# Kernel optimization log

Hardware: AMD Instinct MI355X
Metric: run time of the kernel (lower is better)

Reference implementation:

```python
import jax, jax.numpy as jnp
import numpy as np

HS, WS = 64, 64
SIGMA = 1.2
UPDATE_COEFF = 0.2
R = 3
N_BLOCKS = 3
GROUPS = 8
EPS_GN = 1e-5
CM, CP, CS, CT, HID = 64, 3, 128, 128, 128
B, T, HIN, WIN = 32, 256, 128, 128


def setup_inputs() -> dict:
    key = jax.random.key(0)
    ks = jax.random.split(key, 10)
    s = 0.02
    cin = CM + CP + CT
    f32 = jnp.float32
    return {
        'M': jax.random.normal(ks[0], (B, CM, HIN, WIN), f32),
        'x0_hat_norm': jax.random.uniform(ks[1], (B, T, 2), f32, -1.0, 1.0),
        't_embed': jax.random.normal(ks[2], (B, CT), f32),
        'in_proj_w': jax.random.normal(ks[3], (CS, cin), f32) * s,
        'in_proj_b': jnp.zeros((CS,), f32),
        'rb_c1w': jax.random.normal(ks[4], (N_BLOCKS, CS, CS, 3, 3), f32) * s,
        'rb_c1b': jnp.zeros((N_BLOCKS, CS), f32),
        'rb_g1w': jnp.ones((N_BLOCKS, CS), f32),
        'rb_g1b': jnp.zeros((N_BLOCKS, CS), f32),
        'rb_c2w': jax.random.normal(ks[5], (N_BLOCKS, CS, CS, 3, 3), f32) * s,
        'rb_c2b': jnp.zeros((N_BLOCKS, CS), f32),
        'rb_g2w': jnp.ones((N_BLOCKS, CS), f32),
        'rb_g2b': jnp.zeros((N_BLOCKS, CS), f32),
        'out_w': jax.random.normal(ks[6], (CS, CS), f32) * s,
        'out_b': jnp.zeros((CS,), f32),
        'mlp_w1': jax.random.normal(ks[7], (CS + CT, HID), f32) * s,
        'mlp_b1': jnp.zeros((HID,), f32),
        'mlp_w2': jax.random.normal(ks[8], (HID, HID), f32) * s,
        'mlp_b2': jnp.zeros((HID,), f32),
        'mlp_w3': jax.random.normal(ks[9], (HID, 2), f32) * s,
        'mlp_b3': jnp.zeros((2,), f32),
    }


def _resize_bilinear(M, Hs, Ws):
    # torch F.interpolate bilinear, align_corners=False, no antialias
    Bn, C, H, W = M.shape
    def coords(n_out, n_in):
        sc = n_in / n_out
        c = (jnp.arange(n_out, dtype=M.dtype) + 0.5) * sc - 0.5
        c = jnp.clip(c, 0.0, n_in - 1.0)
        i0 = jnp.floor(c)
        f = c - i0
        i0 = i0.astype(jnp.int32)
        i1 = jnp.minimum(i0 + 1, n_in - 1)
        return i0, i1, f
    y0, y1, fy = coords(Hs, H)
    x0, x1, fx = coords(Ws, W)
    top = M[:, :, y0, :] * (1 - fy)[None, None, :, None] + M[:, :, y1, :] * fy[None, None, :, None]
    return top[:, :, :, x0] * (1 - fx)[None, None, None, :] + top[:, :, :, x1] * fx[None, None, None, :]


def _rasterize_vel(pts, H, W, sigma):
    # pts: (B,T,2) pixel coords -> (B,3,H,W) [heat, vx, vy]
    xs = jnp.arange(W, dtype=pts.dtype)
    ys = jnp.arange(H, dtype=pts.dtype)
    d2 = (pts[:, :, None, None, 0] - xs[None, None, None, :]) ** 2 \
       + (pts[:, :, None, None, 1] - ys[None, None, :, None]) ** 2  # (B,T,H,W)
    w = jnp.exp(-0.5 * d2 / (sigma ** 2 + 1e-8))
    heat = w.max(axis=1)
    v = jnp.pad(jnp.diff(pts, axis=1), ((0, 0), (1, 0), (0, 0)))
    vx = (w * v[:, :, None, None, 0]).sum(axis=1)
    vy = (w * v[:, :, None, None, 1]).sum(axis=1)
    wsum = jnp.maximum(w.sum(axis=1), 1e-6)
    return jnp.stack([heat, vx / wsum, vy / wsum], axis=1)


def _conv3x3(x, w, b):
    y = jax.lax.conv_general_dilated(x, w, (1, 1), 'SAME', dimension_numbers=('NCHW', 'OIHW', 'NCHW'))
    return y + b[None, :, None, None]


def _gn(x, g, b):
    Bn, C, H, W = x.shape
    xr = x.reshape(Bn, GROUPS, C // GROUPS, H, W)
    mu = xr.mean(axis=(2, 3, 4), keepdims=True)
    var = xr.var(axis=(2, 3, 4), keepdims=True)
    xn = ((xr - mu) * jax.lax.rsqrt(var + EPS_GN)).reshape(Bn, C, H, W)
    return xn * g[None, :, None, None] + b[None, :, None, None]


def _grid_sample(S, coords):
    # bilinear, align_corners=False, zero padding. coords (B,T,2) in [-1,1] -> (B,T,C)
    Bn, C, H, W = S.shape
    Tn = coords.shape[1]
    x = ((coords[..., 0] + 1.0) * W - 1.0) * 0.5
    y = ((coords[..., 1] + 1.0) * H - 1.0) * 0.5
    x0 = jnp.floor(x)
    y0 = jnp.floor(y)
    wx = x - x0
    wy = y - y0
    Sf = S.reshape(Bn, C, H * W)
    out = jnp.zeros((Bn, C, Tn), S.dtype)
    for xi, yi, wgt in ((x0, y0, (1 - wx) * (1 - wy)), (x0 + 1, y0, wx * (1 - wy)),
                        (x0, y0 + 1, (1 - wx) * wy), (x0 + 1, y0 + 1, wx * wy)):
        valid = (xi >= 0) & (xi <= W - 1) & (yi >= 0) & (yi <= H - 1)
        xc = jnp.clip(xi, 0, W - 1).astype(jnp.int32)
        yc = jnp.clip(yi, 0, H - 1).astype(jnp.int32)
        idx = jnp.broadcast_to((yc * W + xc)[:, None, :], (Bn, C, Tn))
        g = jnp.take_along_axis(Sf, idx, axis=2)
        out = out + g * (wgt * valid)[:, None, :]
    return out.transpose(0, 2, 1)


def _forward(M, x0_hat_norm, t_embed, in_proj_w, in_proj_b, rb_c1w, rb_c1b, rb_g1w, rb_g1b,
             rb_c2w, rb_c2b, rb_g2w, rb_g2b, out_w, out_b,
             mlp_w1, mlp_b1, mlp_w2, mlp_b2, mlp_w3, mlp_b3):
    Bn = M.shape[0]
    Ms = _resize_bilinear(M, HS, WS)
    t_map = jnp.broadcast_to(t_embed[:, :, None, None], (Bn, CT, HS, WS))
    x = x0_hat_norm
    for _ in range(R):
        x_pix = jnp.stack([(x[..., 0] + 1) * 0.5 * (WS - 1), (x[..., 1] + 1) * 0.5 * (HS - 1)], axis=-1)
        P = _rasterize_vel(x_pix, HS, WS, SIGMA)  # (B,3,HS,WS)
        # SpatialRefine
        inp = jnp.concatenate([Ms, P, t_map], axis=1)
        S = jnp.einsum('bihw,oi->bohw', inp, in_proj_w) + in_proj_b[None, :, None, None]
        for i in range(N_BLOCKS):
            h = jax.nn.silu(_gn(_conv3x3(S, rb_c1w[i], rb_c1b[i]), rb_g1w[i], rb_g1b[i]))
            h = _gn(_conv3x3(h, rb_c2w[i], rb_c2b[i]), rb_g2w[i], rb_g2b[i])
            S = jax.nn.silu(S + h)
        S = jnp.einsum('bihw,oi->bohw', S, out_w) + out_b[None, :, None, None]
        # PointCorrector
        read = _grid_sample(S, x)  # (B,T,CS)
        t_tok = jnp.broadcast_to(t_embed[:, None, :], (Bn, read.shape[1], CT))
        feat = jnp.concatenate([read, t_tok], axis=-1)
        h = jax.nn.silu(feat @ mlp_w1 + mlp_b1)
        h = jax.nn.silu(h @ mlp_w2 + mlp_b2)
        dx = h @ mlp_w3 + mlp_b3
        x = jnp.clip(x + UPDATE_COEFF * dx, -1.0, 1.0)
    return x


def reference(M, x0_hat_norm, t_embed, in_proj_w, in_proj_b, rb_c1w, rb_c1b, rb_g1w, rb_g1b,
              rb_c2w, rb_c2b, rb_g2w, rb_g2b, out_w, out_b,
              mlp_w1, mlp_b1, mlp_w2, mlp_b2, mlp_w3, mlp_b3):
    return _forward(M, x0_hat_norm, t_embed, in_proj_w, in_proj_b, rb_c1w, rb_c1b, rb_g1w, rb_g1b,
                    rb_c2w, rb_c2b, rb_g2w, rb_g2b, out_w, out_b,
                    mlp_w1, mlp_b1, mlp_w2, mlp_b2, mlp_w3, mlp_b3)
```

## Files before the change

kernel.cpp:

```cpp
#include <hip/hip_runtime.h>
#include <cstddef>

#define BN 32
#define TN 256
#define PW 68
#define PLANE 4488

typedef __attribute__((ext_vector_type(8))) short bf16x8;
typedef __attribute__((ext_vector_type(4))) float f32x4;

struct __attribute__((aligned(16))) U4 { unsigned x, y, z, w; };

__device__ __forceinline__ float silu_f(float v) { return v / (1.f + __expf(-v)); }

__device__ __forceinline__ unsigned short f2bf(float f) {
  unsigned u = __float_as_uint(f);
  unsigned r = (u + 0x7fffu + ((u >> 16) & 1u)) >> 16;
  return (unsigned short)r;
}
__device__ __forceinline__ float bf2f(unsigned short h) {
  return __uint_as_float((unsigned)h << 16);
}
__device__ __forceinline__ unsigned pack2(float a, float b) {
  return (unsigned)f2bf(a) | ((unsigned)f2bf(b) << 16);
}

__device__ __forceinline__ void gld16(const unsigned short* g, unsigned short* l) {
  __builtin_amdgcn_global_load_lds((const __attribute__((address_space(1))) unsigned int*)g,
                                   (__attribute__((address_space(3))) unsigned int*)l, 16, 0, 0);
}

__global__ __launch_bounds__(256) void copy_kernel(const float* __restrict__ src, float* __restrict__ dst, int n) {
  int i = blockIdx.x * 256 + threadIdx.x;
  if (i < n) dst[i] = src[i];
}

__global__ __launch_bounds__(256) void zstats_kernel(float* __restrict__ s) {
  int i = blockIdx.x * 256 + threadIdx.x;
  if (i < 18 * 512) s[i] = 0.f;
}

__global__ __launch_bounds__(256) void zerohalo_kernel(unsigned short* __restrict__ base) {
  int idx = blockIdx.x * 256 + threadIdx.x;
  if (idx >= 384 * 1568) return;
  int p = idx / 1568, rem = idx % 1568;
  int hp = rem >> 2, icq = rem & 3;
  int row, x;
  if (hp < 68) { row = 0; x = hp; }
  else if (hp < 136) { row = 65; x = hp - 68; }
  else {
    int i = hp - 136;
    row = 1 + (i >> 2);
    const int cols[4] = {0, 1, 66, 67};
    x = cols[i & 3];
  }
  U4 z = {0u, 0u, 0u, 0u};
  *(U4*)&base[((size_t)p * PLANE + row * PW + x) * 32 + icq * 8] = z;
}

__global__ __launch_bounds__(256) void resize_t_kernel(const float* __restrict__ M, unsigned short* __restrict__ Ms4) {
  __shared__ unsigned short lt[4 * 64 * 72];
  int b = blockIdx.y, yt = blockIdx.x;
  int tid = threadIdx.x;
  for (int i = tid; i < 4 * 64 * 64; i += 256) {
    int c = i >> 8, y = (i >> 6) & 3, x = i & 63;
    const float* p = M + (((size_t)(b * 64 + c) * 128) + (yt * 4 + y) * 2) * 128 + 2 * x;
    float2 a = *(const float2*)p;
    float2 bq = *(const float2*)(p + 128);
    lt[(y * 64 + x) * 72 + c] = f2bf(0.25f * (a.x + a.y + bq.x + bq.y));
  }
  __syncthreads();
  for (int i = tid; i < 2048; i += 256) {
    int icq = i & 3, pxl = (i >> 2) & 255, cc = i >> 10;
    U4 q = *(const U4*)&lt[pxl * 72 + cc * 32 + icq * 8];
    int y = yt * 4 + (pxl >> 6), x = pxl & 63;
    *(U4*)&Ms4[(((size_t)(b * 2 + cc) * PLANE) + (size_t)(y + 1) * PW + x + 2) * 32 + icq * 8] = q;
  }
}

__global__ __launch_bounds__(256) void wprep_kernel(const float* __restrict__ Wsrc, unsigned short* __restrict__ Wdst) {
  int idx = blockIdx.x * 256 + threadIdx.x;
  if (idx >= 147456) return;
  int icp = idx & 31;
  int oc = (idx >> 5) & 127;
  int tc = idx >> 12;
  int t = tc >> 2, cch = tc & 3;
  Wdst[idx] = f2bf(Wsrc[(size_t)oc * 1152 + (size_t)(cch * 32 + icp) * 9 + t]);
}

__global__ __launch_bounds__(256) void wprep_in_kernel(const float* __restrict__ ipw, unsigned short* __restrict__ wi) {
  int idx = blockIdx.x * 256 + threadIdx.x;
  if (idx >= 12288) return;
  int icp = idx & 31, oc = (idx >> 5) & 127, cc = idx >> 12;
  float f = 0.f;
  if (cc < 2) f = ipw[oc * 195 + cc * 32 + icp];
  else if (icp < 3) f = ipw[oc * 195 + 64 + icp];
  wi[idx] = f2bf(f);
}

__global__ __launch_bounds__(256) void wprep_out_kernel(const float* __restrict__ ow, unsigned short* __restrict__ wo) {
  int idx = blockIdx.x * 256 + threadIdx.x;
  if (idx >= 16384) return;
  int icp = idx & 31, oc = (idx >> 5) & 127, cc = idx >> 12;
  wo[idx] = f2bf(ow[oc * 128 + cc * 32 + icp]);
}

__global__ __launch_bounds__(256) void tctr_kernel(const float* __restrict__ w, const float* __restrict__ bias,
                                                   const float* __restrict__ te, float* __restrict__ tctr) {
  int i = blockIdx.x * 256 + threadIdx.x;
  if (i >= BN * 128) return;
  int b = i >> 7, o = i & 127;
  float acc = bias[o];
  const float* wp = w + (size_t)o * 195 + 67;
  const float* t = te + b * 128;
  #pragma unroll 8
  for (int k = 0; k < 128; ++k) acc += wp[k] * t[k];
  tctr[i] = acc;
}

__global__ __launch_bounds__(256) void tpart_kernel(const float* __restrict__ w1, const float* __restrict__ b1,
                                                    const float* __restrict__ te, float* __restrict__ tp) {
  int i = blockIdx.x * 256 + threadIdx.x;
  if (i >= BN * 128) return;
  int b = i >> 7, j = i & 127;
  float acc = b1[j];
  #pragma unroll 8
  for (int k = 0; k < 128; ++k) acc += te[b * 128 + k] * w1[(size_t)(128 + k) * 128 + j];
  tp[i] = acc;
}

__global__ __launch_bounds__(256) void raster4_kernel(const float* __restrict__ x, unsigned short* __restrict__ Pp) {
  int b = blockIdx.y, blk = blockIdx.x;
  int tid = threadIdx.x;
  int pix = blk * 256 + tid;
  __shared__ float spx[TN], spy[TN];
  __shared__ unsigned short lp[256 * 32];
  spx[tid] = (x[(b * TN + tid) * 2] + 1.f) * 0.5f * 63.f;
  spy[tid] = (x[(b * TN + tid) * 2 + 1] + 1.f) * 0.5f * 63.f;
  __syncthreads();
  float fx = (float)(pix & 63), fy = (float)(pix >> 6);
  const float coef = -0.5f / (1.44f + 1e-8f);
  float heat = 0.f, sx = 0.f, sy = 0.f, sw = 0.f;
  float prevx = 0.f, prevy = 0.f;
  for (int t = 0; t < TN; ++t) {
    float px = spx[t], py = spy[t];
    float ddx = px - fx, ddy = py - fy;
    float w = __expf(coef * (ddx * ddx + ddy * ddy));
    heat = fmaxf(heat, w);
    float vx = (t == 0) ? 0.f : px - prevx;
    float vy = (t == 0) ? 0.f : py - prevy;
    prevx = px; prevy = py;
    sx += w * vx; sy += w * vy; sw += w;
  }
  float inv = 1.f / fmaxf(sw, 1e-6f);
  U4 q0; q0.x = pack2(heat, sx * inv); q0.y = pack2(sy * inv, 0.f); q0.z = 0u; q0.w = 0u;
  U4 z = {0u, 0u, 0u, 0u};
  *(U4*)&lp[tid * 32 + 0] = q0;
  *(U4*)&lp[tid * 32 + 8] = z;
  *(U4*)&lp[tid * 32 + 16] = z;
  *(U4*)&lp[tid * 32 + 24] = z;
  __syncthreads();
  for (int it = 0; it < 4; ++it) {
    int sid = it * 256 + tid;
    int pxl = sid >> 2, icq = sid & 3;
    int gp = blk * 256 + pxl;
    int y = gp >> 6, xx = gp & 63;
    *(U4*)&Pp[((size_t)b * PLANE + (size_t)(y + 1) * PW + xx + 2) * 32 + icq * 8] = *(const U4*)&lp[pxl * 32 + icq * 8];
  }
}

__global__ __launch_bounds__(512, 4) void conv3_v6(const unsigned short* __restrict__ In4,
                                                   const unsigned short* __restrict__ Wb,
                                                   const float* __restrict__ Bias,
                                                   float* __restrict__ stOut,
                                                   unsigned short* __restrict__ Out4) {
  __shared__ unsigned short lds[2][13056];
  __shared__ float sred[8][4][2];
  const int P = blockIdx.x;
  const int L = (P & 7) * 64 + (P >> 3);
  const int b = L >> 4, y0 = (L & 15) * 4;
  const int tid = threadIdx.x, l = tid & 63, w = tid >> 6;
  const int ocg = w & 1, rowg = w >> 1, l15 = l & 15, k8 = l >> 4;

  f32x4 acc[4][4];
  #pragma unroll
  for (int mf = 0; mf < 4; ++mf)
    #pragma unroll
    for (int nf = 0; nf < 4; ++nf) acc[mf][nf] = (f32x4){0.f, 0.f, 0.f, 0.f};

  auto issue_stage = [&](int cc, int nb) {
    const unsigned short* slab = In4 + (((size_t)(b * 4 + cc)) * PLANE + (size_t)y0 * PW) * 32;
    #pragma unroll
    for (int i = 0; i < 3; ++i) {
      int G = i * 512 + tid;
      int q = G >> 2;
      int r = q / 68;
      int xs = q - r * 68;
      int src = (G & ~3) | ((G & 3) ^ ((xs >> 1) & 3));
      gld16(slab + (size_t)src * 8, &lds[nb][(size_t)(i * 512 + w * 64) * 8]);
    }
    if (tid < 96) {
      int G = 1536 + tid;
      int q = G >> 2;
      int r = q / 68;
      int xs = q - r * 68;
      int src = (G & ~3) | ((G & 3) ^ ((xs >> 1) & 3));
      gld16(slab + (size_t)src * 8, &lds[nb][(size_t)(1536 + w * 64) * 8]);
    }
  };

  issue_stage(0, 0);
  __syncthreads();

  for (int cc = 0; cc < 4; ++cc) {
    const unsigned short* cur = &lds[cc & 1][0];
    if (cc < 3) issue_stage(cc + 1, (cc & 1) ^ 1);
    __builtin_amdgcn_s_setprio(1);
    #pragma unroll
    for (int t = 0; t < 9; ++t) {
      const int ky = t / 3, kx = t - ky * 3;
      bf16x8 a[4];
      #pragma unroll
      for (int mf = 0; mf < 4; ++mf)
        a[mf] = *(const bf16x8*)&Wb[(((size_t)(t * 4 + cc) * 128) + ocg * 64 + mf * 16 + l15) * 32 + k8 * 8];
      #pragma unroll
      for (int nf = 0; nf < 4; ++nf) {
        int col = nf * 16 + l15 + kx + 1;
        int slot = ((rowg + ky) * 68 + col) * 4 + (k8 ^ ((col >> 1) & 3));
        bf16x8 bv = *(const bf16x8*)&cur[(size_t)slot * 8];
        #pragma unroll
        for (int mf = 0; mf < 4; ++mf)
          acc[mf][nf] = __builtin_amdgcn_mfma_f32_16x16x32_bf16(a[mf], bv, acc[mf][nf], 0, 0, 0);
      }
    }
    __builtin_amdgcn_s_setprio(0);
    __syncthreads();
  }

  #pragma unroll
  for (int mf = 0; mf < 4; ++mf) {
    int oc = ocg * 64 + mf * 16 + k8 * 4;
    float4 bv4 = *(const float4*)&Bias[oc];
    float s = 0.f, qq = 0.f;
    #pragma unroll
    for (int nf = 0; nf < 4; ++nf) {
      float v0 = acc[mf][nf][0] + bv4.x;
      float v1 = acc[mf][nf][1] + bv4.y;
      float v2 = acc[mf][nf][2] + bv4.z;
      float v3 = acc[mf][nf][3] + bv4.w;
      s += (v0 + v1) + (v2 + v3);
      qq += (v0 * v0 + v1 * v1) + (v2 * v2 + v3 * v3);
    }
    #pragma unroll
    for (int off = 32; off > 0; off >>= 1) {
      s += __shfl_xor(s, off, 64);
      qq += __shfl_xor(qq, off, 64);
    }
    if (l == 0) { sred[w][mf][0] = s; sred[w][mf][1] = qq; }
  }
  __syncthreads();
  if (tid < 8) {
    int g = tid, og = g >> 2, mf = g & 3;
    float s = (sred[og][mf][0] + sred[og + 2][mf][0]) + (sred[og + 4][mf][0] + sred[og + 6][mf][0]);
    float qq = (sred[og][mf][1] + sred[og + 2][mf][1]) + (sred[og + 4][mf][1] + sred[og + 6][mf][1]);
    atomicAdd(&stOut[(b * 8 + g) * 2], s);
    atomicAdd(&stOut[(b * 8 + g) * 2 + 1], qq);
  }

  unsigned short* eb = &lds[0][0];
  #pragma unroll
  for (int h = 0; h < 2; ++h) {
    if ((rowg >> 1) == h) {
      int prow = rowg & 1;
      #pragma unroll
      for (int mf = 0; mf < 4; ++mf) {
        int oc = ocg * 64 + mf * 16 + k8 * 4;
        float4 bv4 = *(const float4*)&Bias[oc];
        #pragma unroll
        for (int nf = 0; nf < 4; ++nf) {
          int pxl = prow * 64 + nf * 16 + l15;
          unsigned lo = pack2(acc[mf][nf][0] + bv4.x, acc[mf][nf][1] + bv4.y);
          unsigned hi = pack2(acc[mf][nf][2] + bv4.z, acc[mf][nf][3] + bv4.w);
          unsigned off = (unsigned)(pxl * 256 + oc * 2) ^ ((pxl & 7) << 4);
          *(uint2*)((char*)eb + off) = make_uint2(lo, hi);
        }
      }
    }
    __syncthreads();
    {
      int pxl = tid >> 2, icq = tid & 3;
      int px = h * 128 + pxl;
      int yy = px >> 6, xx = px & 63;
      #pragma unroll
      for (int cc2 = 0; cc2 < 4; ++cc2) {
        unsigned off = (unsigned)(pxl * 256 + cc2 * 64 + icq * 16) ^ ((pxl & 7) << 4);
        U4 q = *(const U4*)((char*)eb + off);
        *(U4*)&Out4[(((size_t)(b * 4 + cc2)) * PLANE + (size_t)(y0 + yy + 1) * PW + xx + 2) * 32 + icq * 8] = q;
      }
    }
    __syncthreads();
  }
}

__global__ __launch_bounds__(256, 2) void conv1_v2(const unsigned short* __restrict__ srcA, int ncA,
                                                   const unsigned short* __restrict__ srcB, int nc,
                                                   const unsigned short* __restrict__ Wb,
                                                   const float* __restrict__ Bias, int perB,
                                                   unsigned short* __restrict__ Out4) {
  __shared__ unsigned short lds[32768];
  const int P = blockIdx.x;
  const int L = (P & 7) * 64 + (P >> 3);
  const int b = L >> 4, px0 = (L & 15) * 256;
  const int tid = threadIdx.x, l = tid & 63, w = tid >> 6;
  const int ocg = w & 1, rowg = w >> 1, l15 = l & 15, k8 = l >> 4;

  f32x4 acc[4][8];
  #pragma unroll
  for (int mf = 0; mf < 4; ++mf)
    #pragma unroll
    for (int nf = 0; nf < 8; ++nf) acc[mf][nf] = (f32x4){0.f, 0.f, 0.f, 0.f};

  for (int cc = 0; cc < nc; ++cc) {
    const unsigned short* base = (cc < ncA) ? srcA + ((size_t)(b * ncA + cc)) * PLANE * 32
                                            : srcB + ((size_t)b) * PLANE * 32;
    bf16x8 a[4];
    #pragma unroll
    for (int mf = 0; mf < 4; ++mf)
      a[mf] = *(const bf16x8*)&Wb[(((size_t)cc * 128) + ocg * 64 + mf * 16 + l15) * 32 + k8 * 8];
    #pragma unroll
    for (int nf = 0; nf < 8; ++nf) {
      int px = px0 + rowg * 128 + nf * 16 + l15;
      int y = px >> 6, x = px & 63;
      bf16x8 bv = *(const bf16x8*)&base[((size_t)(y + 1) * PW + x + 2) * 32 + k8 * 8];
      #pragma unroll
      for (int mf = 0; mf < 4; ++mf)
        acc[mf][nf] = __builtin_amdgcn_mfma_f32_16x16x32_bf16(a[mf], bv, acc[mf][nf], 0, 0, 0);
    }
  }
  const float* bp = Bias + (perB ? b * 128 : 0);
  #pragma unroll
  for (int mf = 0; mf < 4; ++mf) {
    int oc = ocg * 64 + mf * 16 + k8 * 4;
    float4 bv4 = *(const float4*)&bp[oc];
    #pragma unroll
    for (int nf = 0; nf < 8; ++nf) {
      int pxl = rowg * 128 + nf * 16 + l15;
      unsigned lo = pack2(acc[mf][nf][0] + bv4.x, acc[mf][nf][1] + bv4.y);
      unsigned hi = pack2(acc[mf][nf][2] + bv4.z, acc[mf][nf][3] + bv4.w);
      unsigned off = (unsigned)(pxl * 256 + oc * 2) ^ ((pxl & 7) << 4);
      *(uint2*)((char*)lds + off) = make_uint2(lo, hi);
    }
  }
  __syncthreads();
  #pragma unroll
  for (int cc2 = 0; cc2 < 4; ++cc2)
    #pragma unroll
    for (int it = 0; it < 4; ++it) {
      int sid = it * 256 + tid;
      int pxl = sid >> 2, icq = sid & 3;
      unsigned off = (unsigned)(pxl * 256 + cc2 * 64 + icq * 16) ^ ((pxl & 7) << 4);
      U4 q = *(const U4*)((char*)lds + off);
      int px = px0 + pxl;
      int yy = px >> 6, xx = px & 63;
      *(U4*)&Out4[(((size_t)(b * 4 + cc2)) * PLANE + (size_t)(yy + 1) * PW + xx + 2) * 32 + icq * 8] = q;
    }
}

__global__ __launch_bounds__(256) void gn1apply_kernel(unsigned short* __restrict__ A,
                                                       const float* __restrict__ st, const float* __restrict__ gam,
                                                       const float* __restrict__ bet) {
  size_t e8 = (size_t)blockIdx.x * 256 + threadIdx.x;
  int icq = (int)(e8 & 3), x = (int)((e8 >> 2) & 63), y = (int)((e8 >> 8) & 63);
  int cc = (int)((e8 >> 14) & 3), b = (int)(e8 >> 16);
  size_t off = (((size_t)(b * 4 + cc)) * PLANE + (size_t)(y + 1) * PW + x + 2) * 32 + icq * 8;
  int ch = icq * 8;
  int g = cc * 2 + (ch >> 4);
  const float invn = 1.f / 65536.f;
  float ssum = st[(b * 8 + g) * 2], qsum = st[(b * 8 + g) * 2 + 1];
  float mu = ssum * invn;
  float ri = rsqrtf(qsum * invn - mu * mu + 1e-5f);
  int c0 = cc * 32 + ch;
  float4 g0 = *(const float4*)&gam[c0], g1 = *(const float4*)&gam[c0 + 4];
  float4 b0 = *(const float4*)&bet[c0], b1 = *(const float4*)&bet[c0 + 4];
  float gv[8] = {g0.x, g0.y, g0.z, g0.w, g1.x, g1.y, g1.z, g1.w};
  float bv[8] = {b0.x, b0.y, b0.z, b0.w, b1.x, b1.y, b1.z, b1.w};
  U4 va = *(const U4*)&A[off];
  unsigned aa[4] = {va.x, va.y, va.z, va.w};
  unsigned out[4];
  #pragma unroll
  for (int p = 0; p < 4; ++p) {
    float h0 = (bf2f((unsigned short)(aa[p] & 0xffffu)) - mu) * ri * gv[2 * p] + bv[2 * p];
    float h1 = (bf2f((unsigned short)(aa[p] >> 16)) - mu) * ri * gv[2 * p + 1] + bv[2 * p + 1];
    out[p] = pack2(silu_f(h0), silu_f(h1));
  }
  U4 q; q.x = out[0]; q.y = out[1]; q.z = out[2]; q.w = out[3];
  *(U4*)&A[off] = q;
}

__global__ __launch_bounds__(256) void gn2add4_kernel(unsigned short* __restrict__ S, const unsigned short* __restrict__ Bb,
                                                      const float* __restrict__ st, const float* __restrict__ gam,
                                                      const float* __restrict__ bet) {
  size_t e8 = (size_t)blockIdx.x * 256 + threadIdx.x;
  int icq = (int)(e8 & 3), x = (int)((e8 >> 2) & 63), y = (int)((e8 >> 8) & 63);
  int cc = (int)((e8 >> 14) & 3), b = (int)(e8 >> 16);
  size_t off = (((size_t)(b * 4 + cc)) * PLANE + (size_t)(y + 1) * PW + x + 2) * 32 + icq * 8;
  int ch = icq * 8;
  int g = cc * 2 + (ch >> 4);
  const float invn = 1.f / 65536.f;
  float ssum = st[(b * 8 + g) * 2], qsum = st[(b * 8 + g) * 2 + 1];
  float mu = ssum * invn;
  float ri = rsqrtf(qsum * invn - mu * mu + 1e-5f);
  int c0 = cc * 32 + ch;
  float4 g0 = *(const float4*)&gam[c0], g1 = *(const float4*)&gam[c0 + 4];
  float4 b0 = *(const float4*)&bet[c0], b1 = *(const float4*)&bet[c0 + 4];
  float gv[8] = {g0.x, g0.y, g0.z, g0.w, g1.x, g1.y, g1.z, g1.w};
  float bv[8] = {b0.x, b0.y, b0.z, b0.w, b1.x, b1.y, b1.z, b1.w};
  U4 vb = *(const U4*)&Bb[off];
  U4 vs = *(const U4*)&S[off];
  unsigned ab[4] = {vb.x, vb.y, vb.z, vb.w};
  unsigned as[4] = {vs.x, vs.y, vs.z, vs.w};
  unsigned out[4];
  #pragma unroll
  for (int p = 0; p < 4; ++p) {
    float h0 = (bf2f((unsigned short)(ab[p] & 0xffffu)) - mu) * ri * gv[2 * p] + bv[2 * p];
    float h1 = (bf2f((unsigned short)(ab[p] >> 16)) - mu) * ri * gv[2 * p + 1] + bv[2 * p + 1];
    float r0 = silu_f(bf2f((unsigned short)(as[p] & 0xffffu)) + h0);
    float r1 = silu_f(bf2f((unsigned short)(as[p] >> 16)) + h1);
    out[p] = pack2(r0, r1);
  }
  U4 q; q.x = out[0]; q.y = out[1]; q.z = out[2]; q.w = out[3];
  *(U4*)&S[off] = q;
}

__global__ __launch_bounds__(128) void gsample4_kernel(const unsigned short* __restrict__ S2, const float* __restrict__ x,
                                                       float* __restrict__ rd) {
  int token = blockIdx.x, c = threadIdx.x, b = token >> 8;
  float cx = x[token * 2], cy = x[token * 2 + 1];
  float fx = (cx + 1.f) * 32.f - 0.5f;
  float fy = (cy + 1.f) * 32.f - 0.5f;
  float x0f = floorf(fx), y0f = floorf(fy);
  float wx = fx - x0f, wy = fy - y0f;
  const unsigned short* Sb = S2 + ((size_t)(b * 4 + (c >> 5)) * PLANE) * 32 + (c & 31);
  float acc = 0.f;
  #pragma unroll
  for (int cor = 0; cor < 4; ++cor) {
    float xi = x0f + (float)(cor & 1), yi = y0f + (float)(cor >> 1);
    float wgt = ((cor & 1) ? wx : 1.f - wx) * ((cor >> 1) ? wy : 1.f - wy);
    if (xi >= 0.f && xi <= 63.f && yi >= 0.f && yi <= 63.f)
      acc += bf2f(Sb[(size_t)(((int)yi + 1) * PW + (int)xi + 2) * 32]) * wgt;
  }
  rd[(size_t)token * 128 + c] = acc;
}

__global__ __launch_bounds__(256) void mlp_fc_kernel(const float* __restrict__ in, const float* __restrict__ w,
                                                     const float* __restrict__ init, int initPerB,
                                                     float* __restrict__ out) {
  int tok0 = blockIdx.x * 2;
  int tid = threadIdx.x;
  __shared__ float sr[2][128];
  sr[tid >> 7][tid & 127] = in[(size_t)tok0 * 128 + tid];
  __syncthreads();
  int t = tid >> 7, j = tid & 127;
  int token = tok0 + t;
  int b = token >> 8;
  float acc = initPerB ? init[b * 128 + j] : init[j];
  #pragma unroll 8
  for (int k = 0; k < 128; ++k) acc += sr[t][k] * w[(size_t)k * 128 + j];
  out[(size_t)token * 128 + j] = silu_f(acc);
}

__global__ __launch_bounds__(256) void mlp3_update_kernel(const float* __restrict__ h2, const float* __restrict__ w3,
                                                          const float* __restrict__ b3, float* __restrict__ x) {
  int token = blockIdx.x * 256 + threadIdx.x;
  if (token >= BN * TN) return;
  float d0 = b3[0], d1 = b3[1];
  const float* h = h2 + (size_t)token * 128;
  #pragma unroll 8
  for (int k = 0; k < 128; ++k) { float hv = h[k]; d0 += hv * w3[k * 2]; d1 += hv * w3[k * 2 + 1]; }
  float nx = x[token * 2] + 0.2f * d0;
  float ny = x[token * 2 + 1] + 0.2f * d1;
  x[token * 2] = fminf(fmaxf(nx, -1.f), 1.f);
  x[token * 2 + 1] = fminf(fmaxf(ny, -1.f), 1.f);
}

extern "C" void kernel_launch(void* const* d_in, const int* in_sizes, int n_in,
                              void* d_out, int out_size, void* d_ws, size_t ws_size,
                              hipStream_t stream) {
  const float* M   = (const float*)d_in[0];
  const float* x0  = (const float*)d_in[1];
  const float* te  = (const float*)d_in[2];
  const float* ipw = (const float*)d_in[3];
  const float* ipb = (const float*)d_in[4];
  const float* c1w = (const float*)d_in[5];
  const float* c1b = (const float*)d_in[6];
  const float* g1w = (const float*)d_in[7];
  const float* g1b = (const float*)d_in[8];
  const float* c2w = (const float*)d_in[9];
  const float* c2b = (const float*)d_in[10];
  const float* g2w = (const float*)d_in[11];
  const float* g2b = (const float*)d_in[12];
  const float* ow  = (const float*)d_in[13];
  const float* ob  = (const float*)d_in[14];
  const float* w1  = (const float*)d_in[15];
  const float* b1  = (const float*)d_in[16];
  const float* w2  = (const float*)d_in[17];
  const float* b2  = (const float*)d_in[18];
  const float* w3  = (const float*)d_in[19];
  const float* b3  = (const float*)d_in[20];

  const size_t PSH = (size_t)PLANE * 32;
  float* f     = (float*)d_ws;
  float* wx    = f;
  float* tctr  = wx + 16384;
  float* tpart = tctr + 4096;
  float* stats = tpart + 4096;
  float* rd    = stats + 9216;
  float* h1    = rd + 1048576;
  float* h2    = h1 + 1048576;
  unsigned short* S4  = (unsigned short*)(h2 + 1048576);
  unsigned short* A4  = S4 + 128 * PSH;
  unsigned short* B4  = A4 + 128 * PSH;
  unsigned short* Ms4 = B4 + 128 * PSH;
  unsigned short* Pp  = Ms4 + 64 * PSH;
  unsigned short* wc  = Pp + 32 * PSH;
  unsigned short* wi  = wc + 884736;
  unsigned short* wo  = wi + 12288;

  copy_kernel<<<64, 256, 0, stream>>>(x0, wx, 16384);
  zstats_kernel<<<36, 256, 0, stream>>>(stats);
  zerohalo_kernel<<<2352, 256, 0, stream>>>(S4);
  resize_t_kernel<<<dim3(16, 32), 256, 0, stream>>>(M, Ms4);
  tctr_kernel<<<16, 256, 0, stream>>>(ipw, ipb, te, tctr);
  tpart_kernel<<<16, 256, 0, stream>>>(w1, b1, te, tpart);
  for (int i = 0; i < 3; ++i) {
    wprep_kernel<<<576, 256, 0, stream>>>(c1w + (size_t)i * 147456, wc + (size_t)(2 * i) * 147456);
    wprep_kernel<<<576, 256, 0, stream>>>(c2w + (size_t)i * 147456, wc + (size_t)(2 * i + 1) * 147456);
  }
  wprep_in_kernel<<<48, 256, 0, stream>>>(ipw, wi);
  wprep_out_kernel<<<64, 256, 0, stream>>>(ow, wo);

  for (int r = 0; r < 3; ++r) {
    raster4_kernel<<<dim3(16, 32), 256, 0, stream>>>(wx, Pp);
    conv1_v2<<<512, 256, 0, stream>>>(Ms4, 2, Pp, 3, wi, tctr, 1, S4);
    for (int i = 0; i < 3; ++i) {
      float* stA = stats + (size_t)(r * 3 + i) * 512;
      float* stB = stats + (size_t)(9 + r * 3 + i) * 512;
      conv3_v6<<<512, 512, 0, stream>>>(S4, wc + (size_t)(2 * i) * 147456, c1b + i * 128, stA, A4);
      gn1apply_kernel<<<8192, 256, 0, stream>>>(A4, stA, g1w + i * 128, g1b + i * 128);
      conv3_v6<<<512, 512, 0, stream>>>(A4, wc + (size_t)(2 * i + 1) * 147456, c2b + i * 128, stB, B4);
      gn2add4_kernel<<<8192, 256, 0, stream>>>(S4, B4, stB, g2w + i * 128, g2b + i * 128);
    }
    conv1_v2<<<512, 256, 0, stream>>>(S4, 4, nullptr, 4, wo, ob, 0, A4);
    gsample4_kernel<<<8192, 128, 0, stream>>>(A4, wx, rd);
    mlp_fc_kernel<<<4096, 256, 0, stream>>>(rd, w1, tpart, 1, h1);
    mlp_fc_kernel<<<4096, 256, 0, stream>>>(h1, w2, b2, 0, h2);
    mlp3_update_kernel<<<32, 256, 0, stream>>>(h2, w3, b3, wx);
  }
  copy_kernel<<<64, 256, 0, stream>>>(wx, (float*)d_out, 16384);
}
```

Before: 1.725 ms.

## Hoist loop-invariant M projection and fold output 1x1 conv into grid sample

The in-projection contribution of the resized M map, which does not change across refinement rounds, is computed once before the loop into a separate buffer. Each round then adds only the three rasterized channels with a cheap elementwise kernel. The output 1x1 conv is applied only at the sampled token positions, by exploiting linearity of bilinear sampling, instead of over the full 64x64 map. This removes two full-map GEMM-like passes per round, at the cost of an extra buffer and a slightly different rounding order.

```diff
diff --git a/kernel.cpp b/kernel.cpp
--- a/kernel.cpp
+++ b/kernel.cpp
@@ -167,6 +167,41 @@
     int y = gp >> 6, xx = gp & 63;
     *(U4*)&Pp[((size_t)b * PLANE + (size_t)(y + 1) * PW + xx + 2) * 32 + icq * 8] = *(const U4*)&lp[pxl * 32 + icq * 8];
   }
+}
+
+__global__ __launch_bounds__(256) void inproj_fast_kernel(const unsigned short* __restrict__ S0,
+                                                          const unsigned short* __restrict__ Pp,
+                                                          const float* __restrict__ ipw,
+                                                          unsigned short* __restrict__ S) {
+  __shared__ float wp[128][3];
+  int tid = threadIdx.x;
+  if (tid < 128) {
+    wp[tid][0] = ipw[tid * 195 + 64];
+    wp[tid][1] = ipw[tid * 195 + 65];
+    wp[tid][2] = ipw[tid * 195 + 66];
+  }
+  __syncthreads();
+  size_t e8 = (size_t)blockIdx.x * 256 + tid;
+  int icq = (int)(e8 & 3), x = (int)((e8 >> 2) & 63), y = (int)((e8 >> 8) & 63);
+  int cc = (int)((e8 >> 14) & 3), b = (int)(e8 >> 16);
+  size_t off = (((size_t)(b * 4 + cc)) * PLANE + (size_t)(y + 1) * PW + x + 2) * 32 + icq * 8;
+  uint2 p0 = *(const uint2*)&Pp[((size_t)b * PLANE + (size_t)(y + 1) * PW + x + 2) * 32];
+  float h = bf2f((unsigned short)(p0.x & 0xffffu));
+  float vx = bf2f((unsigned short)(p0.x >> 16));
+  float vy = bf2f((unsigned short)(p0.y & 0xffffu));
+  int oc0 = cc * 32 + icq * 8;
+  U4 v0 = *(const U4*)&S0[off];
+  unsigned a[4] = {v0.x, v0.y, v0.z, v0.w};
+  unsigned out[4];
+  #pragma unroll
+  for (int p = 0; p < 4; ++p) {
+    int o0 = oc0 + 2 * p, o1 = oc0 + 2 * p + 1;
+    float r0 = bf2f((unsigned short)(a[p] & 0xffffu)) + h * wp[o0][0] + vx * wp[o0][1] + vy * wp[o0][2];
+    float r1 = bf2f((unsigned short)(a[p] >> 16)) + h * wp[o1][0] + vx * wp[o1][1] + vy * wp[o1][2];
+    out[p] = pack2(r0, r1);
+  }
+  U4 q; q.x = out[0]; q.y = out[1]; q.z = out[2]; q.w = out[3];
+  *(U4*)&S[off] = q;
 }
 
 __global__ __launch_bounds__(512, 4) void conv3_v6(const unsigned short* __restrict__ In4,
@@ -432,24 +467,53 @@
   *(U4*)&S[off] = q;
 }
 
-__global__ __launch_bounds__(128) void gsample4_kernel(const unsigned short* __restrict__ S2, const float* __restrict__ x,
-                                                       float* __restrict__ rd) {
-  int token = blockIdx.x, c = threadIdx.x, b = token >> 8;
-  float cx = x[token * 2], cy = x[token * 2 + 1];
-  float fx = (cx + 1.f) * 32.f - 0.5f;
-  float fy = (cy + 1.f) * 32.f - 0.5f;
-  float x0f = floorf(fx), y0f = floorf(fy);
-  float wx = fx - x0f, wy = fy - y0f;
-  const unsigned short* Sb = S2 + ((size_t)(b * 4 + (c >> 5)) * PLANE) * 32 + (c & 31);
-  float acc = 0.f;
-  #pragma unroll
-  for (int cor = 0; cor < 4; ++cor) {
-    float xi = x0f + (float)(cor & 1), yi = y0f + (float)(cor >> 1);
-    float wgt = ((cor & 1) ? wx : 1.f - wx) * ((cor >> 1) ? wy : 1.f - wy);
-    if (xi >= 0.f && xi <= 63.f && yi >= 0.f && yi <= 63.f)
-      acc += bf2f(Sb[(size_t)(((int)yi + 1) * PW + (int)xi + 2) * 32]) * wgt;
-  }
-  rd[(size_t)token * 128 + c] = acc;
+__global__ __launch_bounds__(256) void gsample_op_kernel(const unsigned short* __restrict__ S4,
+                                                         const float* __restrict__ x,
+                                                         const unsigned short* __restrict__ wo,
+                                                         const float* __restrict__ ob,
+                                                         float* __restrict__ rd) {
+  __shared__ float sv[2][128];
+  int tid = threadIdx.x;
+  int tt = tid >> 7, c = tid & 127;
+  int token = blockIdx.x * 2 + tt;
+  int b = token >> 8;
+  {
+    float cx = x[token * 2], cy = x[token * 2 + 1];
+    float fx = (cx + 1.f) * 32.f - 0.5f;
+    float fy = (cy + 1.f) * 32.f - 0.5f;
+    float x0f = floorf(fx), y0f = floorf(fy);
+    float wx = fx - x0f, wy = fy - y0f;
+    const unsigned short* Sb = S4 + ((size_t)(b * 4 + (c >> 5)) * PLANE) * 32 + (c & 31);
+    float acc = 0.f;
+    #pragma unroll
+    for (int cor = 0; cor < 4; ++cor) {
+      float xi = x0f + (float)(cor & 1), yi = y0f + (float)(cor >> 1);
+      float wgt = ((cor & 1) ? wx : 1.f - wx) * ((cor >> 1) ? wy : 1.f - wy);
+      if (xi >= 0.f && xi <= 63.f && yi >= 0.f && yi <= 63.f)
+        acc += bf2f(Sb[(size_t)(((int)yi + 1) * PW + (int)xi + 2) * 32]) * wgt;
+    }
+    sv[tt][c] = acc;
+  }
+  __syncthreads();
+  {
+    int oc = c;
+    float acc = ob[oc];
+    #pragma unroll
+    for (int cc = 0; cc < 4; ++cc) {
+      #pragma unroll
+      for (int q8 = 0; q8 < 4; ++q8) {
+        U4 wq = *(const U4*)&wo[(size_t)cc * 4096 + oc * 32 + q8 * 8];
+        unsigned a[4] = {wq.x, wq.y, wq.z, wq.w};
+        const float* sp = &sv[tt][cc * 32 + q8 * 8];
+        #pragma unroll
+        for (int p = 0; p < 4; ++p) {
+          acc += bf2f((unsigned short)(a[p] & 0xffffu)) * sp[2 * p];
+          acc += bf2f((unsigned short)(a[p] >> 16)) * sp[2 * p + 1];
+        }
+      }
+    }
+    rd[(size_t)token * 128 + oc] = acc;
+  }
 }
 
 __global__ __launch_bounds__(256) void mlp_fc_kernel(const float* __restrict__ in, const float* __restrict__ w,
@@ -520,7 +584,8 @@
   unsigned short* S4  = (unsigned short*)(h2 + 1048576);
   unsigned short* A4  = S4 + 128 * PSH;
   unsigned short* B4  = A4 + 128 * PSH;
-  unsigned short* Ms4 = B4 + 128 * PSH;
+  unsigned short* S0  = B4 + 128 * PSH;
+  unsigned short* Ms4 = S0 + 128 * PSH;
   unsigned short* Pp  = Ms4 + 64 * PSH;
   unsigned short* wc  = Pp + 32 * PSH;
   unsigned short* wi  = wc + 884736;
@@ -538,10 +603,11 @@
   }
   wprep_in_kernel<<<48, 256, 0, stream>>>(ipw, wi);
   wprep_out_kernel<<<64, 256, 0, stream>>>(ow, wo);
+  conv1_v2<<<512, 256, 0, stream>>>(Ms4, 2, nullptr, 2, wi, tctr, 1, S0);
 
   for (int r = 0; r < 3; ++r) {
     raster4_kernel<<<dim3(16, 32), 256, 0, stream>>>(wx, Pp);
-    conv1_v2<<<512, 256, 0, stream>>>(Ms4, 2, Pp, 3, wi, tctr, 1, S4);
+    inproj_fast_kernel<<<8192, 256, 0, stream>>>(S0, Pp, ipw, S4);
     for (int i = 0; i < 3; ++i) {
       float* stA = stats + (size_t)(r * 3 + i) * 512;
       float* stB = stats + (size_t)(9 + r * 3 + i) * 512;
@@ -550,8 +616,7 @@
       conv3_v6<<<512, 512, 0, stream>>>(A4, wc + (size_t)(2 * i + 1) * 147456, c2b + i * 128, stB, B4);
       gn2add4_kernel<<<8192, 256, 0, stream>>>(S4, B4, stB, g2w + i * 128, g2b + i * 128);
     }
-    conv1_v2<<<512, 256, 0, stream>>>(S4, 4, nullptr, 4, wo, ob, 0, A4);
-    gsample4_kernel<<<8192, 128, 0, stream>>>(A4, wx, rd);
+    gsample_op_kernel<<<4096, 256, 0, stream>>>(S4, wx, wo, ob, rd);
     mlp_fc_kernel<<<4096, 256, 0, stream>>>(rd, w1, tpart, 1, h1);
     mlp_fc_kernel<<<4096, 256, 0, stream>>>(h1, w2, b2, 0, h2);
     mlp3_update_kernel<<<32, 256, 0, stream>>>(h2, w3, b3, wx);
```

New measurement: 1.729 ms, median of 2. Within noise of the previous version (+0.2%).
